# Kernel tuning notes

Measured on AMD Instinct MI355X. Metric: run time of the kernel, lower is better.

## Reference

```python
import jax, jax.numpy as jnp
import numpy as np


def setup_inputs() -> dict:
    key = jax.random.key(0)
    k1, k2, k3, k4 = jax.random.split(key, 4)
    N, T, D, H = 64, 512, 512, 512
    x = jax.random.normal(k1, (N, T, D), dtype=jnp.float32)
    h0 = jax.random.normal(k2, (N, H), dtype=jnp.float32)
    Wx = jax.random.normal(k3, (D, 4 * H), dtype=jnp.float32) / np.sqrt(D)
    Wh = jax.random.normal(k4, (H, 4 * H), dtype=jnp.float32) / np.sqrt(H)
    b = jnp.zeros((4 * H,), dtype=jnp.float32)
    return {"x": x, "h0": h0, "Wx": Wx, "Wh": Wh, "b": b}


def _lstm(x, h0, Wx, Wh, b):
    H = h0.shape[1]
    c0 = jnp.zeros_like(h0)
    # precompute input projection for all timesteps: (N,T,4H) -> (T,N,4H)
    xW = jnp.einsum('ntd,dk->tnk', x, Wx) + b

    def step(carry, xw_t):
        prev_h, prev_c = carry
        a = xw_t + prev_h @ Wh  # (N,4H)
        ai, af, ao, ag = jnp.split(a, 4, axis=1)
        i = jax.nn.sigmoid(ai)
        f = jax.nn.sigmoid(af)
        o = jax.nn.sigmoid(ao)
        g = jnp.tanh(ag)
        next_c = f * prev_c + i * g
        next_h = o * jnp.tanh(next_c)
        return (next_h, next_c), next_h

    _, hs = jax.lax.scan(step, (h0, c0), xW)  # hs: (T,N,H)
    return jnp.transpose(hs, (1, 0, 2))  # (N,T,H)


def reference(x, h0, Wx, Wh, b):
    return _lstm(x, h0, Wx, Wh, b)
```

## Files before the change

### kernel.cpp

```cpp
#include <hip/hip_runtime.h>
#include <math.h>

constexpr int T_ = 512;
constexpr int H_ = 512;
constexpr int V_ = 2048;
constexpr int KW_ = 512;

using short8 = __attribute__((ext_vector_type(8))) short;
using f32x4  = __attribute__((ext_vector_type(4))) float;
using u16x8  = __attribute__((ext_vector_type(8))) unsigned short;

constexpr size_t OFF_WXT   = 0;
constexpr size_t OFF_WHT   = 4u * 1024 * 1024;
constexpr size_t OFF_HS    = 8u * 1024 * 1024;
constexpr size_t OFF_CS    = OFF_HS + 256u * 1024;
constexpr size_t OFF_FLAGS = OFF_CS + 128u * 1024;
constexpr size_t OFF_XS    = OFF_FLAGS + 16u * 1024;
constexpr int    NFLAGS    = 4096;

__device__ __forceinline__ void split_bf16(float x, unsigned short& hi, unsigned short& lo) {
    unsigned u  = __builtin_bit_cast(unsigned, x);
    unsigned rh = (u + 0x7fffu + ((u >> 16) & 1u)) >> 16;
    hi = (unsigned short)rh;
    float hf = __builtin_bit_cast(float, rh << 16);
    float l  = x - hf;
    unsigned ul = __builtin_bit_cast(unsigned, l);
    unsigned rl = (ul + 0x7fffu + ((ul >> 16) & 1u)) >> 16;
    lo = (unsigned short)rl;
}

__device__ __forceinline__ float sigm(float x) { return 1.0f / (1.0f + __expf(-x)); }
__device__ __forceinline__ float tanh_fast(float x) {
    float xc = fminf(fmaxf(x, -15.0f), 15.0f);
    float e = __expf(-2.0f * xc);
    return (1.0f - e) / (1.0f + e);
}

__device__ __forceinline__ size_t pidx(int row, int k) {
    return (size_t)((row >> 4) * 16 + (k >> 5)) * 512 + (((k >> 3) & 3) * 16 + (row & 15)) * 8 + (k & 7);
}

__global__ __launch_bounds__(256) void prep_wt(const float* __restrict__ W,
                                               unsigned short* __restrict__ WT_hi,
                                               unsigned short* __restrict__ WT_lo) {
    __shared__ float tile[32][33];
    const int ot = blockIdx.x;
    const int kt = blockIdx.y;
    const int lx = threadIdx.x;
    const int ly = threadIdx.y;
    #pragma unroll
    for (int i = 0; i < 4; ++i) {
        const int k = kt * 32 + ly + i * 8;
        const int o = ot * 32 + lx;
        tile[ly + i * 8][lx] = W[(size_t)k * V_ + o];
    }
    __syncthreads();
    #pragma unroll
    for (int i = 0; i < 4; ++i) {
        const int o = ot * 32 + ly + i * 8;
        const int v = ((o & 511) << 2) | (o >> 9);
        const int kk = kt * 32 + lx;
        unsigned short hi, lo;
        split_bf16(tile[lx][ly + i * 8], hi, lo);
        const size_t d = pidx(v, kk);
        WT_hi[d] = hi;
        WT_lo[d] = lo;
    }
}

__global__ __launch_bounds__(256) void prep_h0(const float* __restrict__ h0,
                                               unsigned short* __restrict__ hs,
                                               float* __restrict__ cs,
                                               int* __restrict__ flags) {
    const int i = blockIdx.x * 256 + threadIdx.x;
    const int n = i >> 9, hd = i & 511;
    unsigned short hi, lo;
    split_bf16(h0[i], hi, lo);
    const size_t d = pidx(n, hd);
    hs[d] = hi;
    hs[32768 + d] = lo;
    cs[i] = 0.0f;
    if (i < NFLAGS) flags[i] = 0;
}

__global__ __launch_bounds__(256) void xsplit(const float* __restrict__ x,
                                              unsigned short* __restrict__ xs,
                                              int c0, int CT) {
    const int gtid = blockIdx.x * 256 + threadIdx.x;
    const size_t xs_lo = (size_t)CT * 32768;
    const int tot = CT * 4096;
    for (int g = gtid; g < tot; g += 65536) {
        const int lane = g & 63;
        const int rtk  = g >> 6;
        const int kblk = rtk & 15;
        const int rt   = rtk >> 4;
        const int mc = lane & 15, kb = lane >> 4;
        const int r = rt * 16 + mc;
        const int tl = r >> 6, n = r & 63;
        const int k0 = kblk * 32 + kb * 8;
        const float* xp = x + ((size_t)n * T_ + (c0 + tl)) * 512 + k0;
        const float4 va = *(const float4*)xp;
        const float4 vb = *(const float4*)(xp + 4);
        unsigned short hh[8], ll[8];
        split_bf16(va.x, hh[0], ll[0]); split_bf16(va.y, hh[1], ll[1]);
        split_bf16(va.z, hh[2], ll[2]); split_bf16(va.w, hh[3], ll[3]);
        split_bf16(vb.x, hh[4], ll[4]); split_bf16(vb.y, hh[5], ll[5]);
        split_bf16(vb.z, hh[6], ll[6]); split_bf16(vb.w, hh[7], ll[7]);
        u16x8 vh = {hh[0],hh[1],hh[2],hh[3],hh[4],hh[5],hh[6],hh[7]};
        u16x8 vl = {ll[0],ll[1],ll[2],ll[3],ll[4],ll[5],ll[6],ll[7]};
        *(u16x8*)(xs + (size_t)g * 8) = vh;
        *(u16x8*)(xs + xs_lo + (size_t)g * 8) = vl;
    }
}

__global__ __launch_bounds__(256, 1) void xw_gemm(const unsigned short* __restrict__ xs,
                                                  const unsigned short* __restrict__ wxt,
                                                  const float* __restrict__ bias,
                                                  float* __restrict__ xw, int CT) {
    const int tid = threadIdx.x;
    const int wid = tid >> 6, lane = tid & 63;
    const int mc = lane & 15, kb = lane >> 4;
    const int gwave = blockIdx.x * 4 + wid;
    const size_t xs_lo = (size_t)CT * 32768;

    __shared__ float ct[4][16][68];

    const int tiles = CT * 128;
    for (int idx = gwave; idx < tiles; idx += 1024) {
        const int mtA = idx >> 5;
        const int ng  = idx & 31;
        const short* pa  = (const short*)xs + (size_t)mtA * 8192 + lane * 8;
        const short* pal = pa + xs_lo;
        const short* pb  = (const short*)wxt + (size_t)(ng * 4) * 8192 + lane * 8;
        f32x4 acc[4] = {};
        #pragma unroll
        for (int ks = 0; ks < 16; ++ks) {
            const short8 Ah = *(const short8*)(pa + ks * 512);
            const short8 Al = *(const short8*)(pal + ks * 512);
            #pragma unroll
            for (int n2 = 0; n2 < 4; ++n2) {
                const short8 bh = *(const short8*)(pb + (size_t)n2 * 8192 + ks * 512);
                const short8 bl = *(const short8*)(pb + 1048576 + (size_t)n2 * 8192 + ks * 512);
                acc[n2] = __builtin_amdgcn_mfma_f32_16x16x32_bf16(Ah, bh, acc[n2], 0, 0, 0);
                acc[n2] = __builtin_amdgcn_mfma_f32_16x16x32_bf16(Al, bh, acc[n2], 0, 0, 0);
                acc[n2] = __builtin_amdgcn_mfma_f32_16x16x32_bf16(Ah, bl, acc[n2], 0, 0, 0);
            }
        }
        #pragma unroll
        for (int n2 = 0; n2 < 4; ++n2) {
            const int v = ng * 64 + n2 * 16 + mc;
            const float bv = bias[((v & 3) << 9) | (v >> 2)];
            #pragma unroll
            for (int j = 0; j < 4; ++j)
                ct[wid][kb * 4 + j][n2 * 16 + mc] = acc[n2][j] + bv;
        }
        #pragma unroll
        for (int s = 0; s < 4; ++s) {
            const int row16 = s * 4 + (lane >> 4);
            const int col4  = (lane & 15) * 4;
            const float4 cv = *(const float4*)&ct[wid][row16][col4];
            *(float4*)(xw + (size_t)(mtA * 16 + row16) * V_ + ng * 64 + col4) = cv;
        }
    }
}

__global__ __launch_bounds__(256, 1) void lstm_chunk(const unsigned short* __restrict__ wht,
                                                     unsigned short* __restrict__ hs,
                                                     float* __restrict__ cs,
                                                     const float* __restrict__ xw,
                                                     float* __restrict__ out,
                                                     int* __restrict__ flags,
                                                     int c0, int CT) {
    const int tid = threadIdx.x;
    const int wid = tid >> 6, lane = tid & 63;
    const int wg = blockIdx.x;

    __shared__ float red[4][64][36];

    short8 Bh[4][2], Bl[4][2];
    #pragma unroll
    for (int ks = 0; ks < 4; ++ks) {
        #pragma unroll
        for (int nt = 0; nt < 2; ++nt) {
            const size_t bo = (size_t)((wg * 2 + nt) * 16 + wid * 4 + ks) * 512 + lane * 8;
            Bh[ks][nt] = *(const short8*)((const short*)wht + bo);
            Bl[ks][nt] = *(const short8*)((const short*)wht + 1048576 + bo);
            asm volatile("" : "+v"(Bh[ks][nt]));
            asm volatile("" : "+v"(Bl[ks][nt]));
        }
    }

    const int r = tid >> 2, qq = tid & 3;
    float creg[2];
    creg[0] = cs[(size_t)r * 512 + wg * 8 + qq];
    creg[1] = cs[(size_t)r * 512 + wg * 8 + qq + 4];
    const size_t hwb = (size_t)((r >> 4) * 16 + (wg >> 2)) * 512 + ((wg & 3) * 16 + (r & 15)) * 8;

    for (int tl = 0; tl < CT; ++tl) {
        const int t = c0 + tl;
        const short* hbase = (const short*)(hs + (size_t)(t & 1) * 65536);

        const float* xwr = xw + ((size_t)tl * 64 + r) * V_ + wg * 32;
        const f32x4 xv0 = *(const f32x4*)(xwr + qq * 4);
        const f32x4 xv1 = *(const f32x4*)(xwr + (qq + 4) * 4);

        f32x4 acc[4][2] = {};
        #pragma unroll
        for (int ks = 0; ks < 4; ++ks) {
            #pragma unroll
            for (int rt = 0; rt < 4; ++rt) {
                const size_t ao = (size_t)(rt * 16 + wid * 4 + ks) * 512 + lane * 8;
                const short8 Ah = *(const short8*)(hbase + ao);
                const short8 Al = *(const short8*)(hbase + 32768 + ao);
                #pragma unroll
                for (int nt = 0; nt < 2; ++nt) {
                    acc[rt][nt] = __builtin_amdgcn_mfma_f32_16x16x32_bf16(Ah, Bh[ks][nt], acc[rt][nt], 0, 0, 0);
                    acc[rt][nt] = __builtin_amdgcn_mfma_f32_16x16x32_bf16(Al, Bh[ks][nt], acc[rt][nt], 0, 0, 0);
                    acc[rt][nt] = __builtin_amdgcn_mfma_f32_16x16x32_bf16(Ah, Bl[ks][nt], acc[rt][nt], 0, 0, 0);
                }
            }
        }
        {
            const int mc = lane & 15, kb = lane >> 4;
            #pragma unroll
            for (int rt = 0; rt < 4; ++rt)
                #pragma unroll
                for (int nt = 0; nt < 2; ++nt)
                    #pragma unroll
                    for (int j = 0; j < 4; ++j)
                        red[wid][rt * 16 + kb * 4 + j][nt * 16 + mc] = acc[rt][nt][j];
        }
        __syncthreads();

        {
            float* op = out + ((size_t)r * T_ + t) * H_ + wg * 8;
            unsigned short* hdst = hs + (size_t)((t + 1) & 1) * 65536 + hwb;
            #pragma unroll
            for (int half = 0; half < 2; ++half) {
                const int q = qq + half * 4;
                float a[4];
                #pragma unroll
                for (int c2 = 0; c2 < 4; ++c2)
                    a[c2] = red[0][r][q * 4 + c2] + red[1][r][q * 4 + c2]
                          + red[2][r][q * 4 + c2] + red[3][r][q * 4 + c2];
                const f32x4 xv = half ? xv1 : xv0;
                const float iv = sigm(a[0] + xv[0]);
                const float fv = sigm(a[1] + xv[1]);
                const float ov = sigm(a[2] + xv[2]);
                const float gv = tanh_fast(a[3] + xv[3]);
                const float cc = fv * creg[half] + iv * gv;
                creg[half] = cc;
                const float hv = ov * tanh_fast(cc);
                op[q] = hv;
                unsigned short hh, hl;
                split_bf16(hv, hh, hl);
                hdst[q] = hh;
                hdst[32768 + q] = hl;
            }
        }
        __syncthreads();

        __threadfence();
        __syncthreads();
        if (tid == 0)
            __hip_atomic_store(&flags[wg * 32], t + 1,
                               __ATOMIC_RELAXED, __HIP_MEMORY_SCOPE_AGENT);
        bool mine = true;
        do {
            if (tid < 64) {
                int v = __hip_atomic_load(&flags[tid * 32],
                                          __ATOMIC_RELAXED, __HIP_MEMORY_SCOPE_AGENT);
                mine = (v >= t + 1);
                if (!mine) __builtin_amdgcn_s_sleep(2);
            }
        } while (!__syncthreads_and(mine));
        __builtin_amdgcn_fence(__ATOMIC_ACQUIRE, "agent");
        __syncthreads();
    }

    cs[(size_t)r * 512 + wg * 8 + qq]     = creg[0];
    cs[(size_t)r * 512 + wg * 8 + qq + 4] = creg[1];
}

extern "C" void kernel_launch(void* const* d_in, const int* in_sizes, int n_in,
                              void* d_out, int out_size, void* d_ws, size_t ws_size,
                              hipStream_t stream) {
    const float* x  = (const float*)d_in[0];
    const float* h0 = (const float*)d_in[1];
    const float* Wx = (const float*)d_in[2];
    const float* Wh = (const float*)d_in[3];
    const float* b  = (const float*)d_in[4];
    float* out = (float*)d_out;

    char* ws = (char*)d_ws;
    unsigned short* wxt = (unsigned short*)(ws + OFF_WXT);
    unsigned short* wht = (unsigned short*)(ws + OFF_WHT);
    unsigned short* hs  = (unsigned short*)(ws + OFF_HS);
    float* cs           = (float*)(ws + OFF_CS);
    int* flags          = (int*)(ws + OFF_FLAGS);
    unsigned short* xs  = (unsigned short*)(ws + OFF_XS);

    int CT = 8;
    const int cands[7] = {512, 256, 128, 64, 32, 16, 8};
    for (int i = 0; i < 7; ++i) {
        size_t need = OFF_XS + (size_t)cands[i] * (131072 + 524288);
        if (need <= ws_size) { CT = cands[i]; break; }
    }
    float* xw = (float*)(ws + OFF_XS + (size_t)CT * 131072);

    prep_wt<<<dim3(64, 16), dim3(32, 8), 0, stream>>>(Wx, wxt, wxt + (size_t)V_ * KW_);
    prep_wt<<<dim3(64, 16), dim3(32, 8), 0, stream>>>(Wh, wht, wht + (size_t)V_ * KW_);
    prep_h0<<<128, 256, 0, stream>>>(h0, hs, cs, flags);

    for (int c0 = 0; c0 < T_; c0 += CT) {
        xsplit<<<256, 256, 0, stream>>>(x, xs, c0, CT);
        xw_gemm<<<256, 256, 0, stream>>>(xs, wxt, b, xw, CT);
        int cc0 = c0, cct = CT;
        void* kwh = (void*)wht; void* khs = (void*)hs; void* kcs = (void*)cs;
        void* kxw = (void*)xw; void* ko = (void*)out; void* kfl = (void*)flags;
        void* args[] = { &kwh, &khs, &kcs, &kxw, &ko, &kfl, &cc0, &cct };
        (void)hipLaunchCooperativeKernel((void*)lstm_chunk, dim3(64), dim3(256), args, 0, stream);
    }
}
```

Measured before the change: 7.248 ms.

## Vectorize LSTM gate epilogue to 128 threads with 64-bit packed stores and cap chunk size

Result: no change. 7.273 ms (+0.4%).

```diff
diff --git a/kernel.cpp b/kernel.cpp
--- a/kernel.cpp
+++ b/kernel.cpp
@@ -8,7 +8,9 @@
 
 using short8 = __attribute__((ext_vector_type(8))) short;
 using f32x4  = __attribute__((ext_vector_type(4))) float;
+using u16x4  = __attribute__((ext_vector_type(4))) unsigned short;
 using u16x8  = __attribute__((ext_vector_type(8))) unsigned short;
+typedef unsigned long long ull;
 
 constexpr size_t OFF_WXT   = 0;
 constexpr size_t OFF_WHT   = 4u * 1024 * 1024;
@@ -190,19 +192,23 @@
         }
     }
 
-    const int r = tid >> 2, qq = tid & 3;
-    float creg[2];
-    creg[0] = cs[(size_t)r * 512 + wg * 8 + qq];
-    creg[1] = cs[(size_t)r * 512 + wg * 8 + qq + 4];
-    const size_t hwb = (size_t)((r >> 4) * 16 + (wg >> 2)) * 512 + ((wg & 3) * 16 + (r & 15)) * 8;
+    const int r2 = tid >> 1, half2 = tid & 1;
+    f32x4 creg = {0.0f, 0.0f, 0.0f, 0.0f};
+    if (tid < 128)
+        creg = *(const f32x4*)(cs + (size_t)r2 * 512 + wg * 8 + half2 * 4);
+    const size_t hwb = (size_t)((r2 >> 4) * 16 + (wg >> 2)) * 512
+                     + ((wg & 3) * 16 + (r2 & 15)) * 8 + half2 * 4;
 
     for (int tl = 0; tl < CT; ++tl) {
         const int t = c0 + tl;
         const short* hbase = (const short*)(hs + (size_t)(t & 1) * 65536);
 
-        const float* xwr = xw + ((size_t)tl * 64 + r) * V_ + wg * 32;
-        const f32x4 xv0 = *(const f32x4*)(xwr + qq * 4);
-        const f32x4 xv1 = *(const f32x4*)(xwr + (qq + 4) * 4);
+        f32x4 xg[4];
+        if (tid < 128) {
+            const float* xwr = xw + ((size_t)tl * 64 + r2) * V_ + wg * 32 + half2 * 16;
+            #pragma unroll
+            for (int i = 0; i < 4; ++i) xg[i] = *(const f32x4*)(xwr + i * 4);
+        }
 
         f32x4 acc[4][2] = {};
         #pragma unroll
@@ -232,31 +238,41 @@
         }
         __syncthreads();
 
-        {
-            float* op = out + ((size_t)r * T_ + t) * H_ + wg * 8;
+        if (tid < 128) {
+            float hv[4];
+            #pragma unroll
+            for (int i = 0; i < 4; ++i) {
+                const int cbase = half2 * 16 + i * 4;
+                f32x4 av = *(const f32x4*)&red[0][r2][cbase];
+                av += *(const f32x4*)&red[1][r2][cbase];
+                av += *(const f32x4*)&red[2][r2][cbase];
+                av += *(const f32x4*)&red[3][r2][cbase];
+                const float iv = sigm(av[0] + xg[i][0]);
+                const float fv = sigm(av[1] + xg[i][1]);
+                const float ov = sigm(av[2] + xg[i][2]);
+                const float gv = tanh_fast(av[3] + xg[i][3]);
+                const float cc = fv * creg[i] + iv * gv;
+                creg[i] = cc;
+                hv[i] = ov * tanh_fast(cc);
+            }
+            ull* op = (ull*)(out + ((size_t)r2 * T_ + t) * H_ + wg * 8 + half2 * 4);
+            double2 od = {0, 0};
+            float2 o01 = {hv[0], hv[1]}, o23 = {hv[2], hv[3]};
+            __hip_atomic_store(op,     __builtin_bit_cast(ull, o01),
+                               __ATOMIC_RELAXED, __HIP_MEMORY_SCOPE_AGENT);
+            __hip_atomic_store(op + 1, __builtin_bit_cast(ull, o23),
+                               __ATOMIC_RELAXED, __HIP_MEMORY_SCOPE_AGENT);
+            (void)od;
+            unsigned short hh[4], hl[4];
+            #pragma unroll
+            for (int i = 0; i < 4; ++i) split_bf16(hv[i], hh[i], hl[i]);
+            u16x4 vh = {hh[0], hh[1], hh[2], hh[3]};
+            u16x4 vl = {hl[0], hl[1], hl[2], hl[3]};
             unsigned short* hdst = hs + (size_t)((t + 1) & 1) * 65536 + hwb;
-            #pragma unroll
-            for (int half = 0; half < 2; ++half) {
-                const int q = qq + half * 4;
-                float a[4];
-                #pragma unroll
-                for (int c2 = 0; c2 < 4; ++c2)
-                    a[c2] = red[0][r][q * 4 + c2] + red[1][r][q * 4 + c2]
-                          + red[2][r][q * 4 + c2] + red[3][r][q * 4 + c2];
-                const f32x4 xv = half ? xv1 : xv0;
-                const float iv = sigm(a[0] + xv[0]);
-                const float fv = sigm(a[1] + xv[1]);
-                const float ov = sigm(a[2] + xv[2]);
-                const float gv = tanh_fast(a[3] + xv[3]);
-                const float cc = fv * creg[half] + iv * gv;
-                creg[half] = cc;
-                const float hv = ov * tanh_fast(cc);
-                op[q] = hv;
-                unsigned short hh, hl;
-                split_bf16(hv, hh, hl);
-                hdst[q] = hh;
-                hdst[32768 + q] = hl;
-            }
+            __hip_atomic_store((ull*)hdst, __builtin_bit_cast(ull, vh),
+                               __ATOMIC_RELAXED, __HIP_MEMORY_SCOPE_AGENT);
+            __hip_atomic_store((ull*)(hdst + 32768), __builtin_bit_cast(ull, vl),
+                               __ATOMIC_RELAXED, __HIP_MEMORY_SCOPE_AGENT);
         }
         __syncthreads();
 
@@ -278,8 +294,8 @@
         __syncthreads();
     }
 
-    cs[(size_t)r * 512 + wg * 8 + qq]     = creg[0];
-    cs[(size_t)r * 512 + wg * 8 + qq + 4] = creg[1];
+    if (tid < 128)
+        *(f32x4*)(cs + (size_t)r2 * 512 + wg * 8 + half2 * 4) = creg;
 }
 
 extern "C" void kernel_launch(void* const* d_in, const int* in_sizes, int n_in,
@@ -301,8 +317,8 @@
     unsigned short* xs  = (unsigned short*)(ws + OFF_XS);
 
     int CT = 8;
-    const int cands[7] = {512, 256, 128, 64, 32, 16, 8};
-    for (int i = 0; i < 7; ++i) {
+    const int cands[5] = {128, 64, 32, 16, 8};
+    for (int i = 0; i < 5; ++i) {
         size_t need = OFF_XS + (size_t)cands[i] * (131072 + 524288);
         if (need <= ws_size) { CT = cands[i]; break; }
     }
```
